# Optimization experiments

Hardware: AMD Instinct MI355X
Metric: run time of the kernel (lower is better)

The kernel has to match this reference:

```python
import jax, jax.numpy as jnp
import numpy as np

B, L, D, H = 2, 256, 256, 4
DH = D // H  # 64


def setup_inputs() -> dict:
    key = jax.random.key(0)
    ks = jax.random.split(key, 20)
    inp = {
        "q": jax.random.normal(ks[0], (B, L, D), jnp.float32),
        "k": jax.random.normal(ks[1], (B, L, D), jnp.float32),
        "v": jax.random.normal(ks[2], (B, L, D), jnp.float32),
        "attn_mask": jnp.zeros((L, L), jnp.float32),  # nonzero => masked
        "key_padding_mask": jnp.zeros((B, L), bool),
        "pitch_rel": jax.random.normal(ks[3], (B, L, L, D), jnp.float32),
        "dur_rel": jax.random.normal(ks[4], (B, L, L, D), jnp.float32),
    }
    scale = 1.0 / np.sqrt(D)
    names = ["Wq", "Wk", "Wv", "fc", "pr", "dr"]
    for i, n in enumerate(names):
        inp[n + "_w"] = jax.random.normal(ks[5 + 2 * i], (D, D), jnp.float32) * scale
        inp[n + "_b"] = jax.random.normal(ks[6 + 2 * i], (D,), jnp.float32) * 0.01
    return inp


def _linear(x, w, b):
    # torch nn.Linear: y = x @ W^T + b
    return jnp.matmul(x, w.T) + b


def reference(q, k, v, attn_mask, key_padding_mask, pitch_rel, dur_rel,
              Wq_w, Wq_b, Wk_w, Wk_b, Wv_w, Wv_b, fc_w, fc_b,
              pr_w, pr_b, dr_w, dr_b):
    Bq, Lq, Dm = q.shape
    Lk = k.shape[1]
    # project and split heads -> (B, H, L, DH)
    def heads(x, w, b):
        return _linear(x, w, b).reshape(Bq, -1, H, DH).transpose(0, 2, 1, 3)
    qh, kh, vh = heads(q, Wq_w, Wq_b), heads(k, Wk_w, Wk_b), heads(v, Wv_w, Wv_b)

    # content scores: (B, H, Lq, Lk)
    logits = jnp.einsum("bhid,bhjd->bhij", qh, kh)

    # relative pitch bias: pitch_rel (B, Lq, Lk, D) -> (B, Lq, Lk, H, DH)
    pr = _linear(pitch_rel, pr_w, pr_b).reshape(Bq, Lq, Lk, H, DH)
    logits = logits + jnp.einsum("bhid,bijhd->bhij", qh, pr)

    dr = _linear(dur_rel, dr_w, dr_b).reshape(Bq, Lq, Lk, H, DH)
    logits = logits + jnp.einsum("bhid,bijhd->bhij", qh, dr)

    logits = logits / np.sqrt(DH)

    # mask: key_padding_mask broadcast over the QUERY axis (as in source),
    # attn_mask nonzero => masked
    mask = jnp.logical_or(key_padding_mask[:, None, :, None],
                          (attn_mask != 0)[None, None, :, :])
    logits = jnp.where(mask, jnp.float32(-9e15), logits)

    attn = jax.nn.softmax(logits, axis=-1)  # (B, H, Lq, Lk)
    out = jnp.einsum("bhij,bhjd->bhid", attn, vh)  # (B, H, Lq, DH)
    out = out.transpose(0, 2, 1, 3).reshape(Bq, Lq, Dm)
    out = _linear(out, fc_w, fc_b)  # dropout is identity in eval mode
    return out, attn
```

## Files before the change

kernel.cpp:

```cpp
#include <hip/hip_runtime.h>
#include <math.h>


__global__ __launch_bounds__(256) void k_transpose(const float* __restrict__ in,
                                                   float* __restrict__ out) {
  __shared__ float t[32][33];
  int bx = blockIdx.x & 7, by = blockIdx.x >> 3;
  int x = threadIdx.x & 31, y0 = threadIdx.x >> 5;
#pragma unroll
  for (int yy = 0; yy < 32; yy += 8)
    t[yy + y0][x] = in[(size_t)(by * 32 + yy + y0) * 256 + bx * 32 + x];
  __syncthreads();
#pragma unroll
  for (int yy = 0; yy < 32; yy += 8)
    out[(size_t)(bx * 32 + yy + y0) * 256 + by * 32 + x] = t[x][yy + y0];
}

__global__ __launch_bounds__(256) void k_proj(
    const float* __restrict__ q, const float* __restrict__ k_, const float* __restrict__ v,
    const float* __restrict__ Wq, const float* __restrict__ Bq,
    const float* __restrict__ Wk, const float* __restrict__ Bk,
    const float* __restrict__ Wv, const float* __restrict__ Bv,
    float* __restrict__ qh, float* __restrict__ kh, float* __restrict__ vh) {
  int blk = blockIdx.x;
  int m = blk >> 5;
  int r = blk & 31;
  int b = r >> 4, it = (r >> 2) & 3, ot = r & 3;
  const float* X = (m == 0) ? q : (m == 1) ? k_ : v;
  const float* W = (m == 0) ? Wq : (m == 1) ? Wk : Wv;
  const float* Bs = (m == 0) ? Bq : (m == 1) ? Bk : Bv;
  float* OUT = (m == 0) ? qh : (m == 1) ? kh : vh;
  const float scale = (m == 0) ? 0.125f : 1.0f;

  __shared__ float xs[64][33];
  __shared__ float ws[64][33];
  int tid = threadIdx.x;
  int ti = tid >> 4, to = tid & 15;
  int lr = tid >> 2, lc = (tid & 3) * 8;
  float acc[4][4] = {};

  for (int k0 = 0; k0 < 256; k0 += 32) {
    float4 a0 = *(const float4*)(X + (size_t)(b * 256 + it * 64 + lr) * 256 + k0 + lc);
    float4 a1 = *(const float4*)(X + (size_t)(b * 256 + it * 64 + lr) * 256 + k0 + lc + 4);
    xs[lr][lc + 0] = a0.x; xs[lr][lc + 1] = a0.y; xs[lr][lc + 2] = a0.z; xs[lr][lc + 3] = a0.w;
    xs[lr][lc + 4] = a1.x; xs[lr][lc + 5] = a1.y; xs[lr][lc + 6] = a1.z; xs[lr][lc + 7] = a1.w;
    float4 w0 = *(const float4*)(W + (size_t)(ot * 64 + lr) * 256 + k0 + lc);
    float4 w1 = *(const float4*)(W + (size_t)(ot * 64 + lr) * 256 + k0 + lc + 4);
    ws[lr][lc + 0] = w0.x; ws[lr][lc + 1] = w0.y; ws[lr][lc + 2] = w0.z; ws[lr][lc + 3] = w0.w;
    ws[lr][lc + 4] = w1.x; ws[lr][lc + 5] = w1.y; ws[lr][lc + 6] = w1.z; ws[lr][lc + 7] = w1.w;
    __syncthreads();
#pragma unroll
    for (int kk = 0; kk < 32; ++kk) {
      float xv0 = xs[ti * 4 + 0][kk], xv1 = xs[ti * 4 + 1][kk];
      float xv2 = xs[ti * 4 + 2][kk], xv3 = xs[ti * 4 + 3][kk];
      float wv0 = ws[0 * 16 + to][kk], wv1 = ws[1 * 16 + to][kk];
      float wv2 = ws[2 * 16 + to][kk], wv3 = ws[3 * 16 + to][kk];
      acc[0][0] += xv0 * wv0; acc[0][1] += xv0 * wv1; acc[0][2] += xv0 * wv2; acc[0][3] += xv0 * wv3;
      acc[1][0] += xv1 * wv0; acc[1][1] += xv1 * wv1; acc[1][2] += xv1 * wv2; acc[1][3] += xv1 * wv3;
      acc[2][0] += xv2 * wv0; acc[2][1] += xv2 * wv1; acc[2][2] += xv2 * wv2; acc[2][3] += xv2 * wv3;
      acc[3][0] += xv3 * wv0; acc[3][1] += xv3 * wv1; acc[3][2] += xv3 * wv2; acc[3][3] += xv3 * wv3;
    }
    __syncthreads();
  }
#pragma unroll
  for (int ii = 0; ii < 4; ++ii)
#pragma unroll
    for (int oo = 0; oo < 4; ++oo) {
      int i = it * 64 + ti * 4 + ii;
      int dd = oo * 16 + to;
      OUT[(size_t)((b * 4 + ot) * 256 + i) * 64 + dd] = (acc[ii][oo] + Bs[ot * 64 + dd]) * scale;
    }
}

__global__ __launch_bounds__(256) void k_qprdr(
    const float* __restrict__ qh, const float* __restrict__ prw,
    const float* __restrict__ drw, float* __restrict__ qpr, float* __restrict__ qdr) {
  int blk = blockIdx.x;
  int t = blk >> 7;
  int r2 = blk & 127;
  int rt = r2 >> 2, et = r2 & 3;
  const float* W = t ? drw : prw;
  float* OUT = t ? qdr : qpr;
  int h = (rt >> 2) & 3;

  __shared__ float xs[64][33];
  __shared__ float ws2[32][64];
  int tid = threadIdx.x;
  int ti = tid >> 4, to = tid & 15;
  float acc[4][4] = {};

  for (int k0 = 0; k0 < 64; k0 += 32) {
    int lr = tid >> 2, lc = (tid & 3) * 8;
    float4 a0 = *(const float4*)(qh + (size_t)(rt * 64 + lr) * 64 + k0 + lc);
    float4 a1 = *(const float4*)(qh + (size_t)(rt * 64 + lr) * 64 + k0 + lc + 4);
    xs[lr][lc + 0] = a0.x; xs[lr][lc + 1] = a0.y; xs[lr][lc + 2] = a0.z; xs[lr][lc + 3] = a0.w;
    xs[lr][lc + 4] = a1.x; xs[lr][lc + 5] = a1.y; xs[lr][lc + 6] = a1.z; xs[lr][lc + 7] = a1.w;
    int wr = tid >> 3, wc = (tid & 7) * 8;
    float4 w0 = *(const float4*)(W + (size_t)(h * 64 + k0 + wr) * 256 + et * 64 + wc);
    float4 w1 = *(const float4*)(W + (size_t)(h * 64 + k0 + wr) * 256 + et * 64 + wc + 4);
    ws2[wr][wc + 0] = w0.x; ws2[wr][wc + 1] = w0.y; ws2[wr][wc + 2] = w0.z; ws2[wr][wc + 3] = w0.w;
    ws2[wr][wc + 4] = w1.x; ws2[wr][wc + 5] = w1.y; ws2[wr][wc + 6] = w1.z; ws2[wr][wc + 7] = w1.w;
    __syncthreads();
#pragma unroll
    for (int kk = 0; kk < 32; ++kk) {
      float xv0 = xs[ti * 4 + 0][kk], xv1 = xs[ti * 4 + 1][kk];
      float xv2 = xs[ti * 4 + 2][kk], xv3 = xs[ti * 4 + 3][kk];
      float wv0 = ws2[kk][0 * 16 + to], wv1 = ws2[kk][1 * 16 + to];
      float wv2 = ws2[kk][2 * 16 + to], wv3 = ws2[kk][3 * 16 + to];
      acc[0][0] += xv0 * wv0; acc[0][1] += xv0 * wv1; acc[0][2] += xv0 * wv2; acc[0][3] += xv0 * wv3;
      acc[1][0] += xv1 * wv0; acc[1][1] += xv1 * wv1; acc[1][2] += xv1 * wv2; acc[1][3] += xv1 * wv3;
      acc[2][0] += xv2 * wv0; acc[2][1] += xv2 * wv1; acc[2][2] += xv2 * wv2; acc[2][3] += xv2 * wv3;
      acc[3][0] += xv3 * wv0; acc[3][1] += xv3 * wv1; acc[3][2] += xv3 * wv2; acc[3][3] += xv3 * wv3;
    }
    __syncthreads();
  }
#pragma unroll
  for (int ii = 0; ii < 4; ++ii)
#pragma unroll
    for (int oo = 0; oo < 4; ++oo)
      OUT[(size_t)(rt * 64 + ti * 4 + ii) * 256 + et * 64 + oo * 16 + to] = acc[ii][oo];
}

__global__ __launch_bounds__(256) void k_qk(const float* __restrict__ qh,
                                            const float* __restrict__ kh,
                                            float* __restrict__ qk) {
  int blk = blockIdx.x;
  int bh = blk >> 4, it = (blk >> 2) & 3, jt = blk & 3;
  __shared__ float xs[64][33];
  __shared__ float ys[64][33];
  int tid = threadIdx.x;
  int ti = tid >> 4, to = tid & 15;
  float acc[4][4] = {};

  for (int k0 = 0; k0 < 64; k0 += 32) {
    int lr = tid >> 2, lc = (tid & 3) * 8;
    float4 a0 = *(const float4*)(qh + (size_t)(bh * 256 + it * 64 + lr) * 64 + k0 + lc);
    float4 a1 = *(const float4*)(qh + (size_t)(bh * 256 + it * 64 + lr) * 64 + k0 + lc + 4);
    xs[lr][lc + 0] = a0.x; xs[lr][lc + 1] = a0.y; xs[lr][lc + 2] = a0.z; xs[lr][lc + 3] = a0.w;
    xs[lr][lc + 4] = a1.x; xs[lr][lc + 5] = a1.y; xs[lr][lc + 6] = a1.z; xs[lr][lc + 7] = a1.w;
    float4 b0 = *(const float4*)(kh + (size_t)(bh * 256 + jt * 64 + lr) * 64 + k0 + lc);
    float4 b1 = *(const float4*)(kh + (size_t)(bh * 256 + jt * 64 + lr) * 64 + k0 + lc + 4);
    ys[lr][lc + 0] = b0.x; ys[lr][lc + 1] = b0.y; ys[lr][lc + 2] = b0.z; ys[lr][lc + 3] = b0.w;
    ys[lr][lc + 4] = b1.x; ys[lr][lc + 5] = b1.y; ys[lr][lc + 6] = b1.z; ys[lr][lc + 7] = b1.w;
    __syncthreads();
#pragma unroll
    for (int kk = 0; kk < 32; ++kk) {
      float xv0 = xs[ti * 4 + 0][kk], xv1 = xs[ti * 4 + 1][kk];
      float xv2 = xs[ti * 4 + 2][kk], xv3 = xs[ti * 4 + 3][kk];
      float wv0 = ys[0 * 16 + to][kk], wv1 = ys[1 * 16 + to][kk];
      float wv2 = ys[2 * 16 + to][kk], wv3 = ys[3 * 16 + to][kk];
      acc[0][0] += xv0 * wv0; acc[0][1] += xv0 * wv1; acc[0][2] += xv0 * wv2; acc[0][3] += xv0 * wv3;
      acc[1][0] += xv1 * wv0; acc[1][1] += xv1 * wv1; acc[1][2] += xv1 * wv2; acc[1][3] += xv1 * wv3;
      acc[2][0] += xv2 * wv0; acc[2][1] += xv2 * wv1; acc[2][2] += xv2 * wv2; acc[2][3] += xv2 * wv3;
      acc[3][0] += xv3 * wv0; acc[3][1] += xv3 * wv1; acc[3][2] += xv3 * wv2; acc[3][3] += xv3 * wv3;
    }
    __syncthreads();
  }
#pragma unroll
  for (int ii = 0; ii < 4; ++ii)
#pragma unroll
    for (int jj = 0; jj < 4; ++jj)
      qk[(size_t)(bh * 256 + it * 64 + ti * 4 + ii) * 256 + jt * 64 + jj * 16 + to] = acc[ii][jj];
}

__global__ __launch_bounds__(256) void k_bias_softmax(
    const float* __restrict__ pitch, const float* __restrict__ dur,
    const float* __restrict__ qpr, const float* __restrict__ qdr,
    const float* __restrict__ amask, const unsigned char* __restrict__ kpm,
    float* __restrict__ attn) {
  int blk = blockIdx.x;
  int b = blk >> 8, i = blk & 255;
  int tid = threadIdx.x, w = tid >> 6, l = tid & 63;

  __shared__ float logits[4][256];
  __shared__ float mflag[256];

  {
    int hh = tid >> 6, ll = tid & 63;
    float4 qkv = *(const float4*)(attn + (size_t)((b * 4 + hh) * 256 + i) * 256 + 4 * ll);
    *(float4*)&logits[hh][4 * ll] = qkv;
  }
  bool rowmask = kpm[b * 256 + i] != 0;
  mflag[tid] = (rowmask || amask[(size_t)i * 256 + tid] != 0.f) ? 1.f : 0.f;

  float4 qp[4], qd[4];
#pragma unroll
  for (int h = 0; h < 4; ++h) {
    qp[h] = *(const float4*)(qpr + (size_t)((b * 4 + h) * 256 + i) * 256 + 4 * l);
    qd[h] = *(const float4*)(qdr + (size_t)((b * 4 + h) * 256 + i) * 256 + 4 * l);
  }
  __syncthreads();

  const float4* pbase = (const float4*)(pitch + (size_t)(b * 256 + i) * 65536);
  const float4* dbase = (const float4*)(dur + (size_t)(b * 256 + i) * 65536);

  int j = w;
  float4 p = pbase[(size_t)j * 64 + l];
  float4 d4 = dbase[(size_t)j * 64 + l];
  for (int t = 0; t < 64; ++t) {
    float4 pn = make_float4(0.f, 0.f, 0.f, 0.f);
    float4 dn = make_float4(0.f, 0.f, 0.f, 0.f);
    int jn = j + 4;
    if (t < 63) {
      pn = pbase[(size_t)jn * 64 + l];
      dn = dbase[(size_t)jn * 64 + l];
    }
    float s[8];
    s[0] = p.x * qp[0].x + p.y * qp[0].y + p.z * qp[0].z + p.w * qp[0].w;
    s[1] = p.x * qp[1].x + p.y * qp[1].y + p.z * qp[1].z + p.w * qp[1].w;
    s[2] = p.x * qp[2].x + p.y * qp[2].y + p.z * qp[2].z + p.w * qp[2].w;
    s[3] = p.x * qp[3].x + p.y * qp[3].y + p.z * qp[3].z + p.w * qp[3].w;
    s[4] = d4.x * qd[0].x + d4.y * qd[0].y + d4.z * qd[0].z + d4.w * qd[0].w;
    s[5] = d4.x * qd[1].x + d4.y * qd[1].y + d4.z * qd[1].z + d4.w * qd[1].w;
    s[6] = d4.x * qd[2].x + d4.y * qd[2].y + d4.z * qd[2].z + d4.w * qd[2].w;
    s[7] = d4.x * qd[3].x + d4.y * qd[3].y + d4.z * qd[3].z + d4.w * qd[3].w;
#pragma unroll
    for (int m = 1; m <= 4; m <<= 1) {
#pragma unroll
      for (int vv = 0; vv < 8; ++vv) s[vv] += __shfl_xor(s[vv], m);
    }
    int lm = l & 7;
    float a0 = (lm & 1) ? s[1] : s[0];
    float a1 = (lm & 1) ? s[3] : s[2];
    float a2 = (lm & 1) ? s[5] : s[4];
    float a3 = (lm & 1) ? s[7] : s[6];
    float b0 = (lm & 2) ? a1 : a0;
    float b1 = (lm & 2) ? a3 : a2;
    float x = (lm & 4) ? b1 : b0;
    x += __shfl_xor(x, 8);
    x += __shfl_xor(x, 16);
    x += __shfl_xor(x, 32);
    x += __shfl_xor(x, 4);
    if (l < 4) logits[l][j] += x;
    j = jn;
    p = pn;
    d4 = dn;
  }
  __syncthreads();

  int j0 = l * 4;
  float v0 = logits[w][j0 + 0], v1 = logits[w][j0 + 1];
  float v2 = logits[w][j0 + 2], v3 = logits[w][j0 + 3];
  if (mflag[j0 + 0] != 0.f) v0 = -9e15f;
  if (mflag[j0 + 1] != 0.f) v1 = -9e15f;
  if (mflag[j0 + 2] != 0.f) v2 = -9e15f;
  if (mflag[j0 + 3] != 0.f) v3 = -9e15f;
  float mx = fmaxf(fmaxf(v0, v1), fmaxf(v2, v3));
#pragma unroll
  for (int m = 1; m <= 32; m <<= 1) mx = fmaxf(mx, __shfl_xor(mx, m));
  float e0 = __expf(v0 - mx), e1 = __expf(v1 - mx);
  float e2 = __expf(v2 - mx), e3 = __expf(v3 - mx);
  float sm = e0 + e1 + e2 + e3;
#pragma unroll
  for (int m = 1; m <= 32; m <<= 1) sm += __shfl_xor(sm, m);
  float inv = 1.0f / sm;
  float4 rres = make_float4(e0 * inv, e1 * inv, e2 * inv, e3 * inv);
  *(float4*)(attn + (size_t)((b * 4 + w) * 256 + i) * 256 + j0) = rres;
}

__global__ __launch_bounds__(256) void k_pv_fc(
    const float* __restrict__ attn, const float* __restrict__ vh,
    const float* __restrict__ fcT, const float* __restrict__ fcb,
    float* __restrict__ out) {
  int b = blockIdx.x >> 8, i = blockIdx.x & 255;
  int tid = threadIdx.x;
  int h = tid >> 6, l = tid & 63;

  __shared__ float arow[4][256];
  __shared__ float pre[256];

  *(float4*)&arow[h][4 * l] = *(const float4*)(attn + (size_t)((b * 4 + h) * 256 + i) * 256 + 4 * l);
  __syncthreads();

  float acc = 0.f;
  const float* vbase = vh + (size_t)(b * 4 + h) * 256 * 64 + l;
#pragma unroll 4
  for (int jj = 0; jj < 256; ++jj) acc += arow[h][jj] * vbase[(size_t)jj * 64];
  pre[tid] = acc;
  __syncthreads();

  float acc2 = fcb[tid];
#pragma unroll 4
  for (int c = 0; c < 256; ++c) acc2 += pre[c] * fcT[(size_t)c * 256 + tid];
  out[(size_t)(b * 256 + i) * 256 + tid] = acc2;
}

extern "C" void kernel_launch(void* const* d_in, const int* in_sizes, int n_in,
                              void* d_out, int out_size, void* d_ws, size_t ws_size,
                              hipStream_t stream) {
  (void)in_sizes; (void)n_in; (void)out_size; (void)ws_size;
  const float* q = (const float*)d_in[0];
  const float* k = (const float*)d_in[1];
  const float* v = (const float*)d_in[2];
  const float* amask = (const float*)d_in[3];
  const unsigned char* kpm = (const unsigned char*)d_in[4];
  const float* pitch = (const float*)d_in[5];
  const float* dur = (const float*)d_in[6];
  const float* Wq = (const float*)d_in[7];
  const float* Bq = (const float*)d_in[8];
  const float* Wk = (const float*)d_in[9];
  const float* Bk = (const float*)d_in[10];
  const float* Wv = (const float*)d_in[11];
  const float* Bv = (const float*)d_in[12];
  const float* fcw = (const float*)d_in[13];
  const float* fcb = (const float*)d_in[14];
  const float* prw = (const float*)d_in[15];
  const float* drw = (const float*)d_in[17];

  float* out = (float*)d_out;
  float* attn = out + 2 * 256 * 256;

  float* wsf = (float*)d_ws;
  float* qh = wsf;
  float* kh = qh + 131072;
  float* vh = kh + 131072;
  float* qpr = vh + 131072;
  float* qdr = qpr + 524288;
  float* fcT = qdr + 524288;

  k_transpose<<<64, 256, 0, stream>>>(fcw, fcT);
  k_proj<<<96, 256, 0, stream>>>(q, k, v, Wq, Bq, Wk, Bk, Wv, Bv, qh, kh, vh);
  k_qprdr<<<256, 256, 0, stream>>>(qh, prw, drw, qpr, qdr);
  k_qk<<<128, 256, 0, stream>>>(qh, kh, attn);
  k_bias_softmax<<<512, 256, 0, stream>>>(pitch, dur, qpr, qdr, amask, kpm, attn);
  k_pv_fc<<<512, 256, 0, stream>>>(attn, vh, fcT, fcb, out);
}
```

Measured before the change: 121.3 us.

## Split bias-softmax kernel into column-chunked bias kernel and separate softmax

Splits each (b,i) row's bias computation across 4 blocks that each handle 64 key columns, giving 2048 blocks instead of 512 to raise parallelism over the large pitch/dur stream. Pitch and duration dot products are summed before the shuffle reduction, which halves the shuffle work, and the inner loop is unrolled. Softmax moves to its own kernel, adding one launch plus an extra read and write of the attention matrix.

```diff
diff --git a/kernel.cpp b/kernel.cpp
--- a/kernel.cpp
+++ b/kernel.cpp
@@ -163,25 +163,22 @@
       qk[(size_t)(bh * 256 + it * 64 + ti * 4 + ii) * 256 + jt * 64 + jj * 16 + to] = acc[ii][jj];
 }
 
-__global__ __launch_bounds__(256) void k_bias_softmax(
+__global__ __launch_bounds__(256) void k_bias(
     const float* __restrict__ pitch, const float* __restrict__ dur,
     const float* __restrict__ qpr, const float* __restrict__ qdr,
     const float* __restrict__ amask, const unsigned char* __restrict__ kpm,
     float* __restrict__ attn) {
   int blk = blockIdx.x;
-  int b = blk >> 8, i = blk & 255;
+  int jc = blk & 3;
+  int bi = blk >> 2;
+  int b = bi >> 8, i = bi & 255;
   int tid = threadIdx.x, w = tid >> 6, l = tid & 63;
 
-  __shared__ float logits[4][256];
-  __shared__ float mflag[256];
-
-  {
-    int hh = tid >> 6, ll = tid & 63;
-    float4 qkv = *(const float4*)(attn + (size_t)((b * 4 + hh) * 256 + i) * 256 + 4 * ll);
-    *(float4*)&logits[hh][4 * ll] = qkv;
-  }
-  bool rowmask = kpm[b * 256 + i] != 0;
-  mflag[tid] = (rowmask || amask[(size_t)i * 256 + tid] != 0.f) ? 1.f : 0.f;
+  __shared__ float bias_s[4][64];
+
+  size_t rowbase = (size_t)((b * 4 + w) * 256 + i) * 256 + jc * 64;
+  float qkreg = attn[rowbase + l];
+  bool maskreg = (kpm[b * 256 + i] != 0) || (amask[(size_t)i * 256 + jc * 64 + l] != 0.f);
 
   float4 qp[4], qd[4];
 #pragma unroll
@@ -189,73 +186,68 @@
     qp[h] = *(const float4*)(qpr + (size_t)((b * 4 + h) * 256 + i) * 256 + 4 * l);
     qd[h] = *(const float4*)(qdr + (size_t)((b * 4 + h) * 256 + i) * 256 + 4 * l);
   }
-  __syncthreads();
 
   const float4* pbase = (const float4*)(pitch + (size_t)(b * 256 + i) * 65536);
   const float4* dbase = (const float4*)(dur + (size_t)(b * 256 + i) * 65536);
 
-  int j = w;
+  int j = jc * 64 + w;
   float4 p = pbase[(size_t)j * 64 + l];
   float4 d4 = dbase[(size_t)j * 64 + l];
-  for (int t = 0; t < 64; ++t) {
+#pragma unroll 4
+  for (int t = 0; t < 16; ++t) {
     float4 pn = make_float4(0.f, 0.f, 0.f, 0.f);
     float4 dn = make_float4(0.f, 0.f, 0.f, 0.f);
-    int jn = j + 4;
-    if (t < 63) {
-      pn = pbase[(size_t)jn * 64 + l];
-      dn = dbase[(size_t)jn * 64 + l];
-    }
-    float s[8];
-    s[0] = p.x * qp[0].x + p.y * qp[0].y + p.z * qp[0].z + p.w * qp[0].w;
-    s[1] = p.x * qp[1].x + p.y * qp[1].y + p.z * qp[1].z + p.w * qp[1].w;
-    s[2] = p.x * qp[2].x + p.y * qp[2].y + p.z * qp[2].z + p.w * qp[2].w;
-    s[3] = p.x * qp[3].x + p.y * qp[3].y + p.z * qp[3].z + p.w * qp[3].w;
-    s[4] = d4.x * qd[0].x + d4.y * qd[0].y + d4.z * qd[0].z + d4.w * qd[0].w;
-    s[5] = d4.x * qd[1].x + d4.y * qd[1].y + d4.z * qd[1].z + d4.w * qd[1].w;
-    s[6] = d4.x * qd[2].x + d4.y * qd[2].y + d4.z * qd[2].z + d4.w * qd[2].w;
-    s[7] = d4.x * qd[3].x + d4.y * qd[3].y + d4.z * qd[3].z + d4.w * qd[3].w;
-#pragma unroll
-    for (int m = 1; m <= 4; m <<= 1) {
-#pragma unroll
-      for (int vv = 0; vv < 8; ++vv) s[vv] += __shfl_xor(s[vv], m);
-    }
-    int lm = l & 7;
-    float a0 = (lm & 1) ? s[1] : s[0];
-    float a1 = (lm & 1) ? s[3] : s[2];
-    float a2 = (lm & 1) ? s[5] : s[4];
-    float a3 = (lm & 1) ? s[7] : s[6];
-    float b0 = (lm & 2) ? a1 : a0;
-    float b1 = (lm & 2) ? a3 : a2;
-    float x = (lm & 4) ? b1 : b0;
+    if (t < 15) {
+      pn = pbase[(size_t)(j + 4) * 64 + l];
+      dn = dbase[(size_t)(j + 4) * 64 + l];
+    }
+    float s0 = p.x * qp[0].x + p.y * qp[0].y + p.z * qp[0].z + p.w * qp[0].w
+             + d4.x * qd[0].x + d4.y * qd[0].y + d4.z * qd[0].z + d4.w * qd[0].w;
+    float s1 = p.x * qp[1].x + p.y * qp[1].y + p.z * qp[1].z + p.w * qp[1].w
+             + d4.x * qd[1].x + d4.y * qd[1].y + d4.z * qd[1].z + d4.w * qd[1].w;
+    float s2 = p.x * qp[2].x + p.y * qp[2].y + p.z * qp[2].z + p.w * qp[2].w
+             + d4.x * qd[2].x + d4.y * qd[2].y + d4.z * qd[2].z + d4.w * qd[2].w;
+    float s3 = p.x * qp[3].x + p.y * qp[3].y + p.z * qp[3].z + p.w * qp[3].w
+             + d4.x * qd[3].x + d4.y * qd[3].y + d4.z * qd[3].z + d4.w * qd[3].w;
+    s0 += __shfl_xor(s0, 1); s1 += __shfl_xor(s1, 1);
+    s2 += __shfl_xor(s2, 1); s3 += __shfl_xor(s3, 1);
+    s0 += __shfl_xor(s0, 2); s1 += __shfl_xor(s1, 2);
+    s2 += __shfl_xor(s2, 2); s3 += __shfl_xor(s3, 2);
+    int lm = l & 3;
+    float a0 = (lm & 1) ? s1 : s0;
+    float a1 = (lm & 1) ? s3 : s2;
+    float x = (lm & 2) ? a1 : a0;
+    x += __shfl_xor(x, 4);
     x += __shfl_xor(x, 8);
     x += __shfl_xor(x, 16);
     x += __shfl_xor(x, 32);
-    x += __shfl_xor(x, 4);
-    if (l < 4) logits[l][j] += x;
-    j = jn;
+    if (l < 4) bias_s[l][(j & 63)] = x;
+    j += 4;
     p = pn;
     d4 = dn;
   }
   __syncthreads();
 
-  int j0 = l * 4;
-  float v0 = logits[w][j0 + 0], v1 = logits[w][j0 + 1];
-  float v2 = logits[w][j0 + 2], v3 = logits[w][j0 + 3];
-  if (mflag[j0 + 0] != 0.f) v0 = -9e15f;
-  if (mflag[j0 + 1] != 0.f) v1 = -9e15f;
-  if (mflag[j0 + 2] != 0.f) v2 = -9e15f;
-  if (mflag[j0 + 3] != 0.f) v3 = -9e15f;
-  float mx = fmaxf(fmaxf(v0, v1), fmaxf(v2, v3));
+  float val = qkreg + bias_s[w][l];
+  if (maskreg) val = -9e15f;
+  attn[rowbase + l] = val;
+}
+
+__global__ __launch_bounds__(256) void k_softmax(float* __restrict__ attn) {
+  int r = blockIdx.x * 4 + (threadIdx.x >> 6);
+  int l = threadIdx.x & 63;
+  float* row = attn + (size_t)r * 256;
+  float4 v = *(float4*)(row + 4 * l);
+  float mx = fmaxf(fmaxf(v.x, v.y), fmaxf(v.z, v.w));
 #pragma unroll
   for (int m = 1; m <= 32; m <<= 1) mx = fmaxf(mx, __shfl_xor(mx, m));
-  float e0 = __expf(v0 - mx), e1 = __expf(v1 - mx);
-  float e2 = __expf(v2 - mx), e3 = __expf(v3 - mx);
+  float e0 = __expf(v.x - mx), e1 = __expf(v.y - mx);
+  float e2 = __expf(v.z - mx), e3 = __expf(v.w - mx);
   float sm = e0 + e1 + e2 + e3;
 #pragma unroll
   for (int m = 1; m <= 32; m <<= 1) sm += __shfl_xor(sm, m);
   float inv = 1.0f / sm;
-  float4 rres = make_float4(e0 * inv, e1 * inv, e2 * inv, e3 * inv);
-  *(float4*)(attn + (size_t)((b * 4 + w) * 256 + i) * 256 + j0) = rres;
+  *(float4*)(row + 4 * l) = make_float4(e0 * inv, e1 * inv, e2 * inv, e3 * inv);
 }
 
 __global__ __launch_bounds__(256) void k_pv_fc(
@@ -322,6 +314,7 @@
   k_proj<<<96, 256, 0, stream>>>(q, k, v, Wq, Bq, Wk, Bk, Wv, Bv, qh, kh, vh);
   k_qprdr<<<256, 256, 0, stream>>>(qh, prw, drw, qpr, qdr);
   k_qk<<<128, 256, 0, stream>>>(qh, kh, attn);
-  k_bias_softmax<<<512, 256, 0, stream>>>(pitch, dur, qpr, qdr, amask, kpm, attn);
+  k_bias<<<2048, 256, 0, stream>>>(pitch, dur, qpr, qdr, amask, kpm, attn);
+  k_softmax<<<512, 256, 0, stream>>>(attn);
   k_pv_fc<<<512, 256, 0, stream>>>(attn, vh, fcT, fcb, out);
 }
```

New measurement: 118.8 us. -2.1%, faster.
